# Performance work log

Measured on AMD Instinct MI355X. Metric: run time of the kernel, lower is better.

The kernel has to match this reference:

```python
import jax, jax.numpy as jnp
import numpy as np

B, S, D = 2, 2048, 4096
H, KVH = 32, 8
DH = D // H  # 128
N_REP = H // KVH
ROPE_BASE = 10000.0


def _rope_tables(seq_len, d_head, dtype):
    inv_freq = 1.0 / (ROPE_BASE ** (jnp.arange(0, d_head, 2, dtype=jnp.float32) / d_head))
    pos = jnp.arange(seq_len, dtype=jnp.float32)
    freqs = pos[:, None] * inv_freq[None, :]            # (S, DH/2)
    emb = jnp.concatenate([freqs, freqs], axis=-1)       # (S, DH)
    return jnp.cos(emb).astype(dtype), jnp.sin(emb).astype(dtype)


def _rotate_half(x):
    half = x.shape[-1] // 2
    return jnp.concatenate([-x[..., half:], x[..., :half]], axis=-1)


def _apply_rope(x, cos, sin):
    # x: (B, h, S, DH); cos/sin: (S, DH)
    return x * cos[None, None, :, :] + _rotate_half(x) * sin[None, None, :, :]


def setup_inputs() -> dict:
    key = jax.random.key(0)
    ks = jax.random.split(key, 6)
    scale = 0.02
    return {
        "x": jax.random.normal(ks[0], (B, S, D), dtype=jnp.float32),
        "Wq": jax.random.normal(ks[1], (D, H * DH), dtype=jnp.float32) * scale,
        "Wk": jax.random.normal(ks[2], (D, KVH * DH), dtype=jnp.float32) * scale,
        "Wv": jax.random.normal(ks[3], (D, KVH * DH), dtype=jnp.float32) * scale,
        "Wo": jax.random.normal(ks[4], (D, D), dtype=jnp.float32) * scale,
        "bo": jnp.zeros((D,), dtype=jnp.float32),
    }


def reference(x, Wq, Wk, Wv, Wo, bo):
    b, s, _ = x.shape
    # QKV projections (no bias)
    q = (x @ Wq).reshape(b, s, H, DH).transpose(0, 2, 1, 3)    # (B, H, S, DH)
    k = (x @ Wk).reshape(b, s, KVH, DH).transpose(0, 2, 1, 3)  # (B, KVH, S, DH)
    v = (x @ Wv).reshape(b, s, KVH, DH).transpose(0, 2, 1, 3)
    # RoPE on q and k
    cos, sin = _rope_tables(s, DH, x.dtype)
    q = _apply_rope(q, cos, sin)
    k = _apply_rope(k, cos, sin)
    # GQA: repeat KV heads to match query heads
    k = jnp.repeat(k, N_REP, axis=1)  # (B, H, S, DH)
    v = jnp.repeat(v, N_REP, axis=1)
    # Causal scaled dot-product attention
    scale = 1.0 / jnp.sqrt(jnp.asarray(DH, dtype=x.dtype))
    scores = jnp.einsum("bhqd,bhkd->bhqk", q, k) * scale       # (B, H, S, S)
    causal = jnp.tril(jnp.ones((s, s), dtype=bool))
    scores = jnp.where(causal[None, None, :, :], scores, jnp.finfo(x.dtype).min)
    attn = jax.nn.softmax(scores, axis=-1)
    out = jnp.einsum("bhqk,bhkd->bhqd", attn, v)               # (B, H, S, DH)
    out = out.transpose(0, 2, 1, 3).reshape(b, s, H * DH)
    return out @ Wo + bo
```

## Files before the change

### kernel.cpp

```cpp
#include <hip/hip_runtime.h>

typedef unsigned short u16;
typedef unsigned int u32;
typedef __attribute__((ext_vector_type(8))) short s16x8;
typedef __attribute__((ext_vector_type(8))) u16 u16x8;
typedef __attribute__((ext_vector_type(4))) float f32x4;
typedef __attribute__((ext_vector_type(4))) u32 u32x4;

#define SEQ 2048
#define NH 32
#define NKV 8
#define AS1 __attribute__((address_space(1)))
#define AS3 __attribute__((address_space(3)))

__device__ __forceinline__ u16 f2bf(float f) {
  union { float f; u32 u; } v; v.f = f;
  u32 r = v.u + 0x7FFFu + ((v.u >> 16) & 1u);
  return (u16)(r >> 16);
}
__device__ __forceinline__ float bf2f(u16 u) {
  union { u32 u; float f; } v; v.u = ((u32)u) << 16;
  return v.f;
}
__device__ __forceinline__ u32 pack2(float a, float b) {
  return (u32)f2bf(a) | ((u32)f2bf(b) << 16);
}

__global__ void k_conv_bf16(const float* __restrict__ in, u16* __restrict__ out) {
  long i = ((long)blockIdx.x * 256 + threadIdx.x) * 4;
  const float4 v = *(const float4*)&in[i];
  ushort4 ov = { f2bf(v.x), f2bf(v.y), f2bf(v.z), f2bf(v.w) };
  *(ushort4*)&out[i] = ov;
}

__global__ void k_transpose_bf16(const float* __restrict__ W, u16* __restrict__ Wt,
                                 int K, int N) {
  __shared__ u16 T[64 * 65];
  int n0 = blockIdx.x * 64, k0 = blockIdx.y * 64;
  int t = threadIdx.x;
  int cr = t >> 4, cc = (t & 15) * 4;
#pragma unroll
  for (int r2 = 0; r2 < 4; ++r2) {
    int k = cr + r2 * 16;
    const float4 v = *(const float4*)&W[(long)(k0 + k) * N + n0 + cc];
    u16* d = &T[k * 65 + cc];
    d[0] = f2bf(v.x); d[1] = f2bf(v.y); d[2] = f2bf(v.z); d[3] = f2bf(v.w);
  }
  __syncthreads();
#pragma unroll
  for (int r2 = 0; r2 < 4; ++r2) {
    int n = cr + r2 * 16;
    ushort4 ov = { T[(cc + 0) * 65 + n], T[(cc + 1) * 65 + n],
                   T[(cc + 2) * 65 + n], T[(cc + 3) * 65 + n] };
    *(ushort4*)&Wt[(long)(n0 + n) * K + k0 + cc] = ov;
  }
}

__global__ void k_vt(const u16* __restrict__ Vb, u16* __restrict__ Vt) {
  __shared__ u16 T[64][136];
  int s0 = blockIdx.x * 64;
  int g = blockIdx.y;
  const u16* src = Vb + (long)g * SEQ * 128;
  u16* dst = Vt + (long)g * 128 * SEQ;
  int t = threadIdx.x;
#pragma unroll
  for (int i = 0; i < 4; ++i) {
    int c = i * 256 + t;
    int row = c >> 4, col8 = (c & 15) * 8;
    u16x8 v = *(const u16x8*)&src[(long)(s0 + row) * 128 + col8];
#pragma unroll
    for (int j = 0; j < 8; ++j) T[row][col8 + j] = v[j];
  }
  __syncthreads();
#pragma unroll
  for (int i = 0; i < 4; ++i) {
    int c = i * 256 + t;
    int d = c >> 3, k8 = (c & 7) * 8;
    u16x8 v;
#pragma unroll
    for (int j = 0; j < 8; ++j) v[j] = T[k8 + j][d];
    *(u16x8*)&dst[(long)d * SEQ + s0 + k8] = v;
  }
}

__global__ void k_rope_table(float* __restrict__ cosT, float* __restrict__ sinT) {
  int id = blockIdx.x * 256 + threadIdx.x;
  int s = id >> 6, i = id & 63;
  float inv = powf(10000.0f, -(float)i * (1.0f / 64.0f));
  float f = (float)s * inv;
  float sv, cv;
  sincosf(f, &sv, &cv);
  cosT[id] = cv; sinT[id] = sv;
}

__global__ void k_rope_apply(u16* __restrict__ Qb, u16* __restrict__ Kb,
                             const float* __restrict__ cosT, const float* __restrict__ sinT) {
  int id = blockIdx.x * 256 + threadIdx.x;
  int i = id & 63;
  int row = id >> 6;
  u16* base = (row < 131072) ? (Qb + (long)row * 128) : (Kb + (long)(row - 131072) * 128);
  int s = row & (SEQ - 1);
  float c = cosT[s * 64 + i], sn = sinT[s * 64 + i];
  float x0 = bf2f(base[i]), x1 = bf2f(base[i + 64]);
  base[i] = f2bf(x0 * c - x1 * sn);
  base[i + 64] = f2bf(x1 * c + x0 * sn);
}

#define STG2(base_, pl_, ph_, D_)                                                    \
  { __builtin_amdgcn_global_load_lds((const AS1 u32*)((pl_) + (D_)),                 \
        (AS3 u32*)(smem + (base_) + tid * 16), 16, 0, 0);                            \
    __builtin_amdgcn_global_load_lds((const AS1 u32*)((ph_) + (D_)),                 \
        (AS3 u32*)(smem + (base_) + 8192 + tid * 16), 16, 0, 0); }

#define GPHASE(MH, KH, READB, STG_STMT, WAIT_STMT)                                  \
  {                                                                                 \
    const char* Ab_ = smem + cbuf + (KH) * 16384;                                   \
    const char* Bb_ = smem + cbuf + 32768 + (KH) * 16384;                           \
    s16x8 Ar_[4];                                                                   \
    _Pragma("unroll")                                                               \
    for (int m_ = 0; m_ < 4; ++m_)                                                  \
      Ar_[m_] = *(const s16x8*)(Ab_ + aoff + ((MH) * 4 + m_) * 1024);               \
    if (READB) {                                                                    \
      _Pragma("unroll")                                                             \
      for (int n_ = 0; n_ < 4; ++n_)                                                \
        Br[n_] = *(const s16x8*)(Bb_ + boff + n_ * 1024);                           \
    }                                                                               \
    STG_STMT;                                                                       \
    __builtin_amdgcn_s_barrier();                                                   \
    asm volatile("s_waitcnt lgkmcnt(0)" ::: "memory");                              \
    __builtin_amdgcn_sched_barrier(0);                                              \
    __builtin_amdgcn_s_setprio(1);                                                  \
    _Pragma("unroll")                                                               \
    for (int m_ = 0; m_ < 4; ++m_) {                                                \
      _Pragma("unroll")                                                             \
      for (int n_ = 0; n_ < 4; ++n_)                                                \
        acc[(MH) * 4 + m_][n_] = __builtin_amdgcn_mfma_f32_16x16x32_bf16(           \
            Ar_[m_], Br[n_], acc[(MH) * 4 + m_][n_], 0, 0, 0);                      \
    }                                                                               \
    __builtin_amdgcn_s_setprio(0);                                                  \
    WAIT_STMT;                                                                      \
    __builtin_amdgcn_s_barrier();                                                   \
  }

__global__ __launch_bounds__(512, 1) void k_gemm256(
    const u16* __restrict__ A, const u16* __restrict__ Bt,
    u16* __restrict__ Qb, u16* __restrict__ Kb, u16* __restrict__ Vb, int K) {
  extern __shared__ char smem[];
  int bid = blockIdx.x;
  int xc = bid & 7, c = bid >> 3;
  int bm = (xc >> 1) * 4 + c / 12;
  int bn = (xc & 1) * 12 + c % 12;
  int tid = threadIdx.x;
  int lane = tid & 63, wave = tid >> 6;
  int lo = lane & 15, hi = lane >> 4;
  int wm = wave >> 2, wn = wave & 3;
  const u16* Ag = A + (long)bm * 256 * K;
  const u16* Bg = Bt + (long)bn * 256 * K;
  f32x4 zero4 = {0.f, 0.f, 0.f, 0.f};
  f32x4 acc[8][4];
#pragma unroll
  for (int m = 0; m < 8; ++m)
#pragma unroll
    for (int n = 0; n < 4; ++n) acc[m][n] = zero4;

  int aoff = wm * 8192 + ((lo >> 3) << 9) + ((lo & 7) << 4) + (hi << 7);
  int boff = wn * 4096 + ((lo >> 3) << 9) + ((lo & 7) << 4) + (hi << 7);
  int r0 = ((tid >> 5) << 3) + (tid & 7);
  int scol = ((tid >> 3) & 3) << 3;
  const u16* aL = Ag + (long)r0 * K + scol;
  const u16* aH = aL + (long)128 * K;
  const u16* bL = Bg + (long)r0 * K + scol;
  const u16* bH = bL + (long)128 * K;

  int nt = K >> 6;
  STG2(0,             aL, aH, 0);
  STG2(32768,         bL, bH, 0);
  STG2(16384,         aL, aH, 32);
  STG2(49152,         bL, bH, 32);
  STG2(65536,         aL, aH, 64);
  STG2(65536 + 32768, bL, bH, 64);
  asm volatile("s_waitcnt vmcnt(4)" ::: "memory");
  __builtin_amdgcn_s_barrier();

  s16x8 Br[4];
  for (int t = 0; t < nt; ++t) {
    int cbuf = (t & 1) << 16;
    int obuf = cbuf ^ 65536;
    bool s1ok = (t + 1) < nt, s2ok = (t + 2) < nt;
    GPHASE(0, 0, true,
           { if (s1ok) STG2(obuf + 16384, aL, aH, 96); }, {})
    GPHASE(1, 0, false,
           { if (s1ok) STG2(obuf + 49152, bL, bH, 96); }, {})
    GPHASE(0, 1, true,
           { if (s2ok) STG2(cbuf, aL, aH, 128); }, {})
    GPHASE(1, 1, false,
           { if (s2ok) STG2(cbuf + 32768, bL, bH, 128); },
           {
             if (s2ok)      asm volatile("s_waitcnt vmcnt(4)" ::: "memory");
             else if (s1ok) asm volatile("s_waitcnt vmcnt(0)" ::: "memory");
           })
    aL += 64; aH += 64; bL += 64; bH += 64;
  }

#pragma unroll
  for (int mr = 0; mr < 8; ++mr) {
#pragma unroll
    for (int n = 0; n < 4; ++n) {
      int colg = bn * 256 + wn * 64 + n * 16 + lo;
#pragma unroll
      for (int r = 0; r < 4; ++r) {
        int rowg = bm * 256 + wm * 128 + mr * 16 + hi * 4 + r;
        float v = acc[mr][n][r];
        int bb = rowg >> 11, s = rowg & 2047;
        u16 u = f2bf(v);
        int d = colg & 127;
        if (colg < 4096) {
          int hh = colg >> 7;
          Qb[(((long)bb * NH + hh) * SEQ + s) * 128 + d] = u;
        } else if (colg < 5120) {
          int hh = (colg - 4096) >> 7;
          Kb[(((long)bb * NKV + hh) * SEQ + s) * 128 + d] = u;
        } else {
          int hh = (colg - 5120) >> 7;
          Vb[(((long)bb * NKV + hh) * SEQ + s) * 128 + d] = u;
        }
      }
    }
  }
}

__global__ __launch_bounds__(512, 2) void k_gemm128(
    const u16* __restrict__ A, const u16* __restrict__ Bt,
    float* __restrict__ Cf, const float* __restrict__ bias, int K) {
  extern __shared__ char smem[];
  int bid = blockIdx.x;
  int xc = bid & 7, c = bid >> 3;
  int bm = (xc >> 1) * 8 + (c >> 3);
  int bn = (xc & 1) * 8 + (c & 7);
  int tid = threadIdx.x;
  int lane = tid & 63, wave = tid >> 6;
  int lo = lane & 15, hi = lane >> 4;
  int wm = wave >> 2, wn = wave & 3;
  const u16* Ag = A + (long)bm * 128 * K;
  const u16* Bg = Bt + (long)bn * 256 * K;
  f32x4 zero4 = {0.f, 0.f, 0.f, 0.f};
  f32x4 acc[4][4];
#pragma unroll
  for (int m = 0; m < 4; ++m)
#pragma unroll
    for (int n = 0; n < 4; ++n) acc[m][n] = zero4;

  int aoff = wm * 4096 + ((lo >> 3) << 9) + ((lo & 7) << 4) + (hi << 7);
  int boff = 8192 + wn * 4096 + ((lo >> 3) << 9) + ((lo & 7) << 4) + (hi << 7);
  int r0 = ((tid >> 5) << 3) + (tid & 7);
  int scol = ((tid >> 3) & 3) << 3;
  const u16* aP  = Ag + (long)r0 * K + scol;
  const u16* bP0 = Bg + (long)r0 * K + scol;
  const u16* bP1 = bP0 + (long)128 * K;

#define G128STG(nxt_, D_)                                                            \
  { __builtin_amdgcn_global_load_lds((const AS1 u32*)(aP + (D_)),                    \
        (AS3 u32*)(smem + (nxt_) + tid * 16), 16, 0, 0);                             \
    __builtin_amdgcn_global_load_lds((const AS1 u32*)(bP0 + (D_)),                   \
        (AS3 u32*)(smem + (nxt_) + 8192 + tid * 16), 16, 0, 0);                      \
    __builtin_amdgcn_global_load_lds((const AS1 u32*)(bP1 + (D_)),                   \
        (AS3 u32*)(smem + (nxt_) + 16384 + tid * 16), 16, 0, 0); }

  int nt = K >> 5;
  G128STG(0, 0);
  asm volatile("s_waitcnt vmcnt(0)" ::: "memory");
  __builtin_amdgcn_s_barrier();

  for (int t = 0; t < nt; ++t) {
    int cur = (t & 1) * 24576;
    int nxt = cur ^ 24576;
    bool more = (t + 1) < nt;
    if (more) G128STG(nxt, 32);
    s16x8 Af[4], Bf[4];
#pragma unroll
    for (int m = 0; m < 4; ++m) Af[m] = *(const s16x8*)(smem + cur + aoff + m * 1024);
#pragma unroll
    for (int n = 0; n < 4; ++n) Bf[n] = *(const s16x8*)(smem + cur + boff + n * 1024);
    asm volatile("s_waitcnt lgkmcnt(0)" ::: "memory");
    __builtin_amdgcn_sched_barrier(0);
    __builtin_amdgcn_s_setprio(1);
#pragma unroll
    for (int m = 0; m < 4; ++m)
#pragma unroll
      for (int n = 0; n < 4; ++n)
        acc[m][n] = __builtin_amdgcn_mfma_f32_16x16x32_bf16(Af[m], Bf[n], acc[m][n], 0, 0, 0);
    __builtin_amdgcn_s_setprio(0);
    if (more) asm volatile("s_waitcnt vmcnt(0)" ::: "memory");
    __builtin_amdgcn_s_barrier();
    aP += 32; bP0 += 32; bP1 += 32;
  }

#pragma unroll
  for (int m = 0; m < 4; ++m) {
#pragma unroll
    for (int n = 0; n < 4; ++n) {
      int colg = bn * 256 + wn * 64 + n * 16 + lo;
#pragma unroll
      for (int r = 0; r < 4; ++r) {
        int rowg = bm * 128 + wm * 64 + m * 16 + hi * 4 + r;
        Cf[(long)rowg * 4096 + colg] = acc[m][n][r] + bias[colg];
      }
    }
  }
#undef G128STG
}

__device__ __forceinline__ void stage_load(u32x4* kr_, u32x4* vr_,
    const u16* __restrict__ Kg, const u16* __restrict__ Vg, int kt, int tid) {
#pragma unroll
  for (int i = 0; i < 4; ++i) {
    int idx = i * 256 + tid;
    int kr = idx >> 4, kc = idx & 15;
    kr_[i] = *(const u32x4*)&Kg[(long)(kt + kr) * 128 + kc * 8];
    int vr = idx >> 3, vc = idx & 7;
    vr_[i] = *(const u32x4*)&Vg[(long)vr * SEQ + kt + vc * 8];
  }
}
__device__ __forceinline__ void stage_write(const u32x4* kr_, const u32x4* vr_,
    u16* Ks, u16* Vs, int tid) {
  char* KsB = (char*)Ks; char* VsB = (char*)Vs;
#pragma unroll
  for (int i = 0; i < 4; ++i) {
    int idx = i * 256 + tid;
    int kr = idx >> 4, kc = idx & 15;
    *(u32x4*)(KsB + ((kr * 256 + kc * 16) ^ ((kr & 7) << 4))) = kr_[i];
    int vr = idx >> 3, vc = idx & 7;
    *(u32x4*)(VsB + ((vr * 128 + vc * 16) ^ ((vr & 7) << 4))) = vr_[i];
  }
}

__global__ __launch_bounds__(256, 2) void k_attn(
    const u16* __restrict__ Qb, const u16* __restrict__ Kb,
    const u16* __restrict__ Vt, u16* __restrict__ AO) {
  __shared__ u16 Ks0[64 * 128], Ks1[64 * 128], Vs0[128 * 64], Vs1[128 * 64];
  __shared__ u16 Ps[4][2][16][32];
  int gid = blockIdx.x;
  int wid = (gid & 7) * 128 + (gid >> 3);
  int g = wid >> 6, w = wid & 63;
  int b = g >> 3, kvh = g & 7;
  int h = kvh * 4 + (w >> 4);
  int qt = 15 - (w & 15);
  int qb0 = qt * 128;
  int tid = threadIdx.x, lane = tid & 63, wave = tid >> 6;
  int lo = lane & 15, hi = lane >> 4;
  int q0w = qb0 + wave * 32;

  const u16* Kg = Kb + (long)(b * NKV + kvh) * SEQ * 128;
  const u16* Vg = Vt + (long)(b * NKV + kvh) * 128 * SEQ;
  const u16* Qg = Qb + (long)(b * NH + h) * SEQ * 128;

  s16x8 qf[2][4];
#pragma unroll
  for (int qs = 0; qs < 2; ++qs)
#pragma unroll
    for (int ds = 0; ds < 4; ++ds)
      qf[qs][ds] = *(const s16x8*)&Qg[(long)(q0w + qs * 16 + lo) * 128 + ds * 32 + hi * 8];

  f32x4 zero4 = {0.f, 0.f, 0.f, 0.f};
  f32x4 o[2][8];
#pragma unroll
  for (int qs = 0; qs < 2; ++qs)
#pragma unroll
    for (int dt = 0; dt < 8; ++dt) o[qs][dt] = zero4;
  float m_run[2] = {-1e30f, -1e30f};
  float l_run[2] = {0.f, 0.f};
  const float scale = 0.088388347648318447f;

  char* PsQ0 = (char*)&Ps[wave][0][0][0];
  char* PsQ1 = (char*)&Ps[wave][1][0][0];
  int pbase = lo << 6;

  u32x4 kreg[4], vreg[4];
  int ntiles = (qb0 >> 6) + 2;
  stage_load(kreg, vreg, Kg, Vg, 0, tid);
  stage_write(kreg, vreg, Ks0, Vs0, tid);
  __syncthreads();

  for (int t = 0; t < ntiles; ++t) {
    int kt = t << 6;
    u16* Ks = (t & 1) ? Ks1 : Ks0;
    u16* Vs = (t & 1) ? Vs1 : Vs0;
    bool more = (t + 1 < ntiles);
    if (more) stage_load(kreg, vreg, Kg, Vg, (t + 1) << 6, tid);
    if (kt <= q0w + 31) {
      f32x4 sa[2][4];
#pragma unroll
      for (int qs = 0; qs < 2; ++qs)
#pragma unroll
        for (int a = 0; a < 4; ++a) sa[qs][a] = zero4;
#pragma unroll
      for (int ds = 0; ds < 4; ++ds) {
        s16x8 kf[4];
#pragma unroll
        for (int a = 0; a < 4; ++a)
          kf[a] = *(const s16x8*)&Ks[((a * 16 + lo) << 7) + (((ds * 4 + hi) ^ (lo & 7)) << 3)];
#pragma unroll
        for (int qs = 0; qs < 2; ++qs)
#pragma unroll
          for (int a = 0; a < 4; ++a)
            sa[qs][a] = __builtin_amdgcn_mfma_f32_16x16x32_bf16(kf[a], qf[qs][ds], sa[qs][a], 0, 0, 0);
      }
      bool pmask = (kt + 63) > q0w;
      u32 pp[2][4][2];
#pragma unroll
      for (int qs = 0; qs < 2; ++qs) {
        float pv[16];
        int qrow = q0w + qs * 16 + lo;
#pragma unroll
        for (int a = 0; a < 4; ++a)
#pragma unroll
          for (int r = 0; r < 4; ++r) {
            float s = sa[qs][a][r] * scale;
            if (pmask && (kt + a * 16 + hi * 4 + r) > qrow) s = -1e30f;
            pv[a * 4 + r] = s;
          }
        float mx = pv[0];
#pragma unroll
        for (int i = 1; i < 16; ++i) mx = fmaxf(mx, pv[i]);
        mx = fmaxf(mx, __shfl_xor(mx, 16));
        mx = fmaxf(mx, __shfl_xor(mx, 32));
        float mnew = fmaxf(m_run[qs], mx);
        if (!__all(mnew - m_run[qs] <= 8.0f)) {
          float corr = __expf(m_run[qs] - mnew);
          m_run[qs] = mnew;
          l_run[qs] *= corr;
#pragma unroll
          for (int dt = 0; dt < 8; ++dt)
#pragma unroll
            for (int r = 0; r < 4; ++r) o[qs][dt][r] *= corr;
        }
        float sum = 0.f;
#pragma unroll
        for (int i = 0; i < 16; ++i) { pv[i] = __expf(pv[i] - m_run[qs]); sum += pv[i]; }
        sum += __shfl_xor(sum, 16);
        sum += __shfl_xor(sum, 32);
        l_run[qs] += sum;
#pragma unroll
        for (int a = 0; a < 4; ++a) {
          pp[qs][a][0] = pack2(pv[a * 4 + 0], pv[a * 4 + 1]);
          pp[qs][a][1] = pack2(pv[a * 4 + 2], pv[a * 4 + 3]);
        }
      }
#pragma unroll
      for (int kb = 0; kb < 2; ++kb) {
#pragma unroll
        for (int qs = 0; qs < 2; ++qs) {
          char* Pw = qs ? PsQ1 : PsQ0;
#pragma unroll
          for (int al = 0; al < 2; ++al) {
            uint2 wv; wv.x = pp[qs][kb * 2 + al][0]; wv.y = pp[qs][kb * 2 + al][1];
            *(uint2*)(Pw + pbase + (((al * 4 + hi) ^ (lo & 7)) << 3)) = wv;
          }
        }
        asm volatile("s_waitcnt lgkmcnt(0)" ::: "memory");
        __builtin_amdgcn_sched_barrier(0);
        union { uint2 u2[2]; s16x8 v; } bu0, bu1;
        bu0.u2[0] = *(uint2*)(PsQ0 + pbase + (((hi * 2 + 0) ^ (lo & 7)) << 3));
        bu0.u2[1] = *(uint2*)(PsQ0 + pbase + (((hi * 2 + 1) ^ (lo & 7)) << 3));
        bu1.u2[0] = *(uint2*)(PsQ1 + pbase + (((hi * 2 + 0) ^ (lo & 7)) << 3));
        bu1.u2[1] = *(uint2*)(PsQ1 + pbase + (((hi * 2 + 1) ^ (lo & 7)) << 3));
#pragma unroll
        for (int dt = 0; dt < 8; ++dt) {
          s16x8 vf = *(const s16x8*)((char*)Vs +
              (((dt * 16 + lo) * 128 + (kb * 4 + hi) * 16) ^ ((lo & 7) << 4)));
          o[0][dt] = __builtin_amdgcn_mfma_f32_16x16x32_bf16(vf, bu0.v, o[0][dt], 0, 0, 0);
          o[1][dt] = __builtin_amdgcn_mfma_f32_16x16x32_bf16(vf, bu1.v, o[1][dt], 0, 0, 0);
        }
      }
    }
    if (more) stage_write(kreg, vreg, (t & 1) ? Ks0 : Ks1, (t & 1) ? Vs0 : Vs1, tid);
    __syncthreads();
  }

#pragma unroll
  for (int qs = 0; qs < 2; ++qs) {
    float inv = 1.0f / l_run[qs];
    long base = ((long)(b * SEQ + q0w + qs * 16 + lo)) * 4096 + h * 128;
#pragma unroll
    for (int dt = 0; dt < 8; ++dt) {
      uint2 wv;
      wv.x = pack2(o[qs][dt][0] * inv, o[qs][dt][1] * inv);
      wv.y = pack2(o[qs][dt][2] * inv, o[qs][dt][3] * inv);
      *(uint2*)&AO[base + dt * 16 + hi * 4] = wv;
    }
  }
}

extern "C" void kernel_launch(void* const* d_in, const int* in_sizes, int n_in,
                              void* d_out, int out_size, void* d_ws, size_t ws_size,
                              hipStream_t stream) {
  const float* x  = (const float*)d_in[0];
  const float* Wq = (const float*)d_in[1];
  const float* Wk = (const float*)d_in[2];
  const float* Wv = (const float*)d_in[3];
  const float* Wo = (const float*)d_in[4];
  const float* bo = (const float*)d_in[5];
  float* out = (float*)d_out;

  char* ws = (char*)d_ws;
  u16* xb     = (u16*)(ws);
  u16* Wt     = (u16*)(ws + 33554432);
  u16* Vtb    = (u16*)(ws + 67108864);
  u16* Qb     = (u16*)(ws + 83886080);
  u16* Kb     = (u16*)(ws + 117440512);
  u16* Vb     = (u16*)(ws + 125829120);
  float* cosT = (float*)(ws + 134217728);
  float* sinT = (float*)(ws + 134742016);
  if (ws_size < 135266304) return;
  u16* AO  = xb;
  u16* Wto = Wt;

  (void)hipFuncSetAttribute((const void*)k_gemm256,
                            hipFuncAttributeMaxDynamicSharedMemorySize, 131072);

  k_conv_bf16<<<16384, 256, 0, stream>>>(x, xb);
  k_transpose_bf16<<<dim3(64, 64), 256, 0, stream>>>(Wq, Wt, 4096, 4096);
  k_transpose_bf16<<<dim3(16, 64), 256, 0, stream>>>(Wk, Wt + (long)4096 * 4096, 4096, 1024);
  k_transpose_bf16<<<dim3(16, 64), 256, 0, stream>>>(Wv, Wt + (long)5120 * 4096, 4096, 1024);
  k_rope_table<<<512, 256, 0, stream>>>(cosT, sinT);
  k_gemm256<<<384, 512, 131072, stream>>>(xb, Wt, Qb, Kb, Vb, 4096);
  k_vt<<<dim3(32, 16), 256, 0, stream>>>(Vb, Vtb);
  k_rope_apply<<<40960, 256, 0, stream>>>(Qb, Kb, cosT, sinT);
  k_transpose_bf16<<<dim3(64, 64), 256, 0, stream>>>(Wo, Wto, 4096, 4096);
  k_attn<<<1024, 256, 0, stream>>>(Qb, Kb, Vtb, AO);
  k_gemm128<<<512, 512, 49152, stream>>>(AO, Wto, out, bo, 4096);
}
```

Measured before the change: 700.6 us.

## Swap GEMM tile shapes between QKV and output projections, reorder staging

```diff
diff --git a/kernel.cpp b/kernel.cpp
--- a/kernel.cpp
+++ b/kernel.cpp
@@ -106,11 +106,14 @@
   base[i + 64] = f2bf(x1 * c + x0 * sn);
 }
 
-#define STG2(base_, pl_, ph_, D_)                                                    \
+#define STG_B2(base_, pl_, ph_, D_)                                                  \
   { __builtin_amdgcn_global_load_lds((const AS1 u32*)((pl_) + (D_)),                 \
         (AS3 u32*)(smem + (base_) + tid * 16), 16, 0, 0);                            \
     __builtin_amdgcn_global_load_lds((const AS1 u32*)((ph_) + (D_)),                 \
         (AS3 u32*)(smem + (base_) + 8192 + tid * 16), 16, 0, 0); }
+#define STG_A1(base_, p_, D_)                                                        \
+  { __builtin_amdgcn_global_load_lds((const AS1 u32*)((p_) + (D_)),                  \
+        (AS3 u32*)(smem + (base_) + tid * 16), 16, 0, 0); }
 
 #define GPHASE(MH, KH, READB, STG_STMT, WAIT_STMT)                                  \
   {                                                                                 \
@@ -125,10 +128,7 @@
       for (int n_ = 0; n_ < 4; ++n_)                                                \
         Br[n_] = *(const s16x8*)(Bb_ + boff + n_ * 1024);                           \
     }                                                                               \
-    STG_STMT;                                                                       \
     __builtin_amdgcn_s_barrier();                                                   \
-    asm volatile("s_waitcnt lgkmcnt(0)" ::: "memory");                              \
-    __builtin_amdgcn_sched_barrier(0);                                              \
     __builtin_amdgcn_s_setprio(1);                                                  \
     _Pragma("unroll")                                                               \
     for (int m_ = 0; m_ < 4; ++m_) {                                                \
@@ -138,18 +138,19 @@
             Ar_[m_], Br[n_], acc[(MH) * 4 + m_][n_], 0, 0, 0);                      \
     }                                                                               \
     __builtin_amdgcn_s_setprio(0);                                                  \
+    STG_STMT;                                                                       \
     WAIT_STMT;                                                                      \
     __builtin_amdgcn_s_barrier();                                                   \
   }
 
 __global__ __launch_bounds__(512, 1) void k_gemm256(
     const u16* __restrict__ A, const u16* __restrict__ Bt,
-    u16* __restrict__ Qb, u16* __restrict__ Kb, u16* __restrict__ Vb, int K) {
+    float* __restrict__ Cf, const float* __restrict__ bias, int K, int bnP) {
   extern __shared__ char smem[];
   int bid = blockIdx.x;
   int xc = bid & 7, c = bid >> 3;
-  int bm = (xc >> 1) * 4 + c / 12;
-  int bn = (xc & 1) * 12 + c % 12;
+  int bm = (xc >> 1) * 4 + c / bnP;
+  int bn = (xc & 1) * bnP + c % bnP;
   int tid = threadIdx.x;
   int lane = tid & 63, wave = tid >> 6;
   int lo = lane & 15, hi = lane >> 4;
@@ -173,12 +174,12 @@
   const u16* bH = bL + (long)128 * K;
 
   int nt = K >> 6;
-  STG2(0,             aL, aH, 0);
-  STG2(32768,         bL, bH, 0);
-  STG2(16384,         aL, aH, 32);
-  STG2(49152,         bL, bH, 32);
-  STG2(65536,         aL, aH, 64);
-  STG2(65536 + 32768, bL, bH, 64);
+  STG_B2(0,             aL, aH, 0);
+  STG_B2(32768,         bL, bH, 0);
+  STG_B2(16384,         aL, aH, 32);
+  STG_B2(49152,         bL, bH, 32);
+  STG_B2(65536,         aL, aH, 64);
+  STG_B2(65536 + 32768, bL, bH, 64);
   asm volatile("s_waitcnt vmcnt(4)" ::: "memory");
   __builtin_amdgcn_s_barrier();
 
@@ -188,13 +189,13 @@
     int obuf = cbuf ^ 65536;
     bool s1ok = (t + 1) < nt, s2ok = (t + 2) < nt;
     GPHASE(0, 0, true,
-           { if (s1ok) STG2(obuf + 16384, aL, aH, 96); }, {})
+           { if (s1ok) STG_B2(obuf + 16384, aL, aH, 96); }, {})
     GPHASE(1, 0, false,
-           { if (s1ok) STG2(obuf + 49152, bL, bH, 96); }, {})
+           { if (s1ok) STG_B2(obuf + 49152, bL, bH, 96); }, {})
     GPHASE(0, 1, true,
-           { if (s2ok) STG2(cbuf, aL, aH, 128); }, {})
+           { if (s2ok) STG_B2(cbuf, aL, aH, 128); }, {})
     GPHASE(1, 1, false,
-           { if (s2ok) STG2(cbuf + 32768, bL, bH, 128); },
+           { if (s2ok) STG_B2(cbuf + 32768, bL, bH, 128); },
            {
              if (s2ok)      asm volatile("s_waitcnt vmcnt(4)" ::: "memory");
              else if (s1ok) asm volatile("s_waitcnt vmcnt(0)" ::: "memory");
@@ -210,9 +211,94 @@
 #pragma unroll
       for (int r = 0; r < 4; ++r) {
         int rowg = bm * 256 + wm * 128 + mr * 16 + hi * 4 + r;
-        float v = acc[mr][n][r];
+        Cf[(long)rowg * 4096 + colg] = acc[mr][n][r] + bias[colg];
+      }
+    }
+  }
+}
+
+__global__ __launch_bounds__(512, 1) void k_gemm128b(
+    const u16* __restrict__ A, const u16* __restrict__ Bt,
+    u16* __restrict__ Qb, u16* __restrict__ Kb, u16* __restrict__ Vb, int K) {
+  extern __shared__ char smem[];
+  int bid = blockIdx.x;
+  int xc = bid & 7, c = bid >> 3;
+  int bm = (xc >> 1) * 8 + c / 12;
+  int bn = (xc & 1) * 12 + c % 12;
+  int tid = threadIdx.x;
+  int lane = tid & 63, wave = tid >> 6;
+  int lo = lane & 15, hi = lane >> 4;
+  int wm = wave >> 2, wn = wave & 3;
+  const u16* Ag = A + (long)bm * 128 * K;
+  const u16* Bg = Bt + (long)bn * 256 * K;
+  f32x4 zero4 = {0.f, 0.f, 0.f, 0.f};
+  f32x4 acc[4][4];
+#pragma unroll
+  for (int m = 0; m < 4; ++m)
+#pragma unroll
+    for (int n = 0; n < 4; ++n) acc[m][n] = zero4;
+
+  int aoff = wm * 4096 + ((lo >> 3) << 9) + ((lo & 7) << 4) + (hi << 7);
+  int boff = wn * 4096 + ((lo >> 3) << 9) + ((lo & 7) << 4) + (hi << 7);
+  int r0 = ((tid >> 5) << 3) + (tid & 7);
+  int scol = ((tid >> 3) & 3) << 3;
+  const u16* aP = Ag + (long)r0 * K + scol;
+  const u16* bL = Bg + (long)r0 * K + scol;
+  const u16* bH = bL + (long)128 * K;
+
+  int nt = K >> 6;
+  STG_A1(0,             aP, 0);
+  STG_B2(16384,         bL, bH, 0);
+  STG_A1(8192,          aP, 32);
+  STG_B2(32768,         bL, bH, 32);
+  STG_A1(49152,         aP, 64);
+  STG_B2(49152 + 16384, bL, bH, 64);
+  asm volatile("s_waitcnt vmcnt(3)" ::: "memory");
+  __builtin_amdgcn_s_barrier();
+
+  for (int t = 0; t < nt; ++t) {
+    int cbuf = (t & 1) * 49152;
+    int obuf = cbuf ^ 49152;
+    bool s1ok = (t + 1) < nt, s2ok = (t + 2) < nt;
+#pragma unroll
+    for (int KH = 0; KH < 2; ++KH) {
+      const char* Ab_ = smem + cbuf + KH * 8192;
+      const char* Bb_ = smem + cbuf + 16384 + KH * 16384;
+      s16x8 Ar_[4], Br_[4];
+#pragma unroll
+      for (int m_ = 0; m_ < 4; ++m_) Ar_[m_] = *(const s16x8*)(Ab_ + aoff + m_ * 1024);
+#pragma unroll
+      for (int n_ = 0; n_ < 4; ++n_) Br_[n_] = *(const s16x8*)(Bb_ + boff + n_ * 1024);
+      __builtin_amdgcn_s_barrier();
+      __builtin_amdgcn_s_setprio(1);
+#pragma unroll
+      for (int m_ = 0; m_ < 4; ++m_)
+#pragma unroll
+        for (int n_ = 0; n_ < 4; ++n_)
+          acc[m_][n_] = __builtin_amdgcn_mfma_f32_16x16x32_bf16(Ar_[m_], Br_[n_], acc[m_][n_], 0, 0, 0);
+      __builtin_amdgcn_s_setprio(0);
+      if (KH == 0) {
+        if (s1ok) { STG_A1(obuf + 8192, aP, 96); STG_B2(obuf + 32768, bL, bH, 96); }
+      } else {
+        if (s2ok) { STG_A1(cbuf, aP, 128); STG_B2(cbuf + 16384, bL, bH, 128); }
+        if (s2ok)      asm volatile("s_waitcnt vmcnt(3)" ::: "memory");
+        else if (s1ok) asm volatile("s_waitcnt vmcnt(0)" ::: "memory");
+      }
+      __builtin_amdgcn_s_barrier();
+    }
+    aP += 64; bL += 64; bH += 64;
+  }
+
+#pragma unroll
+  for (int m = 0; m < 4; ++m) {
+#pragma unroll
+    for (int n = 0; n < 4; ++n) {
+      int colg = bn * 256 + wn * 64 + n * 16 + lo;
+#pragma unroll
+      for (int r = 0; r < 4; ++r) {
+        int rowg = bm * 128 + wm * 64 + m * 16 + hi * 4 + r;
         int bb = rowg >> 11, s = rowg & 2047;
-        u16 u = f2bf(v);
+        u16 u = f2bf(acc[m][n][r]);
         int d = colg & 127;
         if (colg < 4096) {
           int hh = colg >> 7;
@@ -227,87 +313,6 @@
       }
     }
   }
-}
-
-__global__ __launch_bounds__(512, 2) void k_gemm128(
-    const u16* __restrict__ A, const u16* __restrict__ Bt,
-    float* __restrict__ Cf, const float* __restrict__ bias, int K) {
-  extern __shared__ char smem[];
-  int bid = blockIdx.x;
-  int xc = bid & 7, c = bid >> 3;
-  int bm = (xc >> 1) * 8 + (c >> 3);
-  int bn = (xc & 1) * 8 + (c & 7);
-  int tid = threadIdx.x;
-  int lane = tid & 63, wave = tid >> 6;
-  int lo = lane & 15, hi = lane >> 4;
-  int wm = wave >> 2, wn = wave & 3;
-  const u16* Ag = A + (long)bm * 128 * K;
-  const u16* Bg = Bt + (long)bn * 256 * K;
-  f32x4 zero4 = {0.f, 0.f, 0.f, 0.f};
-  f32x4 acc[4][4];
-#pragma unroll
-  for (int m = 0; m < 4; ++m)
-#pragma unroll
-    for (int n = 0; n < 4; ++n) acc[m][n] = zero4;
-
-  int aoff = wm * 4096 + ((lo >> 3) << 9) + ((lo & 7) << 4) + (hi << 7);
-  int boff = 8192 + wn * 4096 + ((lo >> 3) << 9) + ((lo & 7) << 4) + (hi << 7);
-  int r0 = ((tid >> 5) << 3) + (tid & 7);
-  int scol = ((tid >> 3) & 3) << 3;
-  const u16* aP  = Ag + (long)r0 * K + scol;
-  const u16* bP0 = Bg + (long)r0 * K + scol;
-  const u16* bP1 = bP0 + (long)128 * K;
-
-#define G128STG(nxt_, D_)                                                            \
-  { __builtin_amdgcn_global_load_lds((const AS1 u32*)(aP + (D_)),                    \
-        (AS3 u32*)(smem + (nxt_) + tid * 16), 16, 0, 0);                             \
-    __builtin_amdgcn_global_load_lds((const AS1 u32*)(bP0 + (D_)),                   \
-        (AS3 u32*)(smem + (nxt_) + 8192 + tid * 16), 16, 0, 0);                      \
-    __builtin_amdgcn_global_load_lds((const AS1 u32*)(bP1 + (D_)),                   \
-        (AS3 u32*)(smem + (nxt_) + 16384 + tid * 16), 16, 0, 0); }
-
-  int nt = K >> 5;
-  G128STG(0, 0);
-  asm volatile("s_waitcnt vmcnt(0)" ::: "memory");
-  __builtin_amdgcn_s_barrier();
-
-  for (int t = 0; t < nt; ++t) {
-    int cur = (t & 1) * 24576;
-    int nxt = cur ^ 24576;
-    bool more = (t + 1) < nt;
-    if (more) G128STG(nxt, 32);
-    s16x8 Af[4], Bf[4];
-#pragma unroll
-    for (int m = 0; m < 4; ++m) Af[m] = *(const s16x8*)(smem + cur + aoff + m * 1024);
-#pragma unroll
-    for (int n = 0; n < 4; ++n) Bf[n] = *(const s16x8*)(smem + cur + boff + n * 1024);
-    asm volatile("s_waitcnt lgkmcnt(0)" ::: "memory");
-    __builtin_amdgcn_sched_barrier(0);
-    __builtin_amdgcn_s_setprio(1);
-#pragma unroll
-    for (int m = 0; m < 4; ++m)
-#pragma unroll
-      for (int n = 0; n < 4; ++n)
-        acc[m][n] = __builtin_amdgcn_mfma_f32_16x16x32_bf16(Af[m], Bf[n], acc[m][n], 0, 0, 0);
-    __builtin_amdgcn_s_setprio(0);
-    if (more) asm volatile("s_waitcnt vmcnt(0)" ::: "memory");
-    __builtin_amdgcn_s_barrier();
-    aP += 32; bP0 += 32; bP1 += 32;
-  }
-
-#pragma unroll
-  for (int m = 0; m < 4; ++m) {
-#pragma unroll
-    for (int n = 0; n < 4; ++n) {
-      int colg = bn * 256 + wn * 64 + n * 16 + lo;
-#pragma unroll
-      for (int r = 0; r < 4; ++r) {
-        int rowg = bm * 128 + wm * 64 + m * 16 + hi * 4 + r;
-        Cf[(long)rowg * 4096 + colg] = acc[m][n][r] + bias[colg];
-      }
-    }
-  }
-#undef G128STG
 }
 
 __device__ __forceinline__ void stage_load(u32x4* kr_, u32x4* vr_,
@@ -517,16 +522,18 @@
 
   (void)hipFuncSetAttribute((const void*)k_gemm256,
                             hipFuncAttributeMaxDynamicSharedMemorySize, 131072);
+  (void)hipFuncSetAttribute((const void*)k_gemm128b,
+                            hipFuncAttributeMaxDynamicSharedMemorySize, 98304);
 
   k_conv_bf16<<<16384, 256, 0, stream>>>(x, xb);
   k_transpose_bf16<<<dim3(64, 64), 256, 0, stream>>>(Wq, Wt, 4096, 4096);
   k_transpose_bf16<<<dim3(16, 64), 256, 0, stream>>>(Wk, Wt + (long)4096 * 4096, 4096, 1024);
   k_transpose_bf16<<<dim3(16, 64), 256, 0, stream>>>(Wv, Wt + (long)5120 * 4096, 4096, 1024);
   k_rope_table<<<512, 256, 0, stream>>>(cosT, sinT);
-  k_gemm256<<<384, 512, 131072, stream>>>(xb, Wt, Qb, Kb, Vb, 4096);
+  k_gemm128b<<<768, 512, 98304, stream>>>(xb, Wt, Qb, Kb, Vb, 4096);
   k_vt<<<dim3(32, 16), 256, 0, stream>>>(Vb, Vtb);
   k_rope_apply<<<40960, 256, 0, stream>>>(Qb, Kb, cosT, sinT);
   k_transpose_bf16<<<dim3(64, 64), 256, 0, stream>>>(Wo, Wto, 4096, 4096);
   k_attn<<<1024, 256, 0, stream>>>(Qb, Kb, Vtb, AO);
-  k_gemm128<<<512, 512, 49152, stream>>>(AO, Wto, out, bo, 4096);
-}
+  k_gemm256<<<256, 512, 131072, stream>>>(AO, Wto, out, bo, 4096, 8);
+}
```

Result: faster. 681.1 us (-2.8%).
